# Performance work log

Hardware: AMD Instinct MI355X
Metric: run time of the kernel (lower is better)

## Reference

```python
import jax, jax.numpy as jnp
import numpy as np

G, U, I, D, L = 4, 100000, 50000, 64, 50   # graphNum, users, items, latdim, pos_length
H = 4                                       # attention heads
ATT_LAYERS = 2
SSL = 32
GNN_LAYER = 2
LEAKY = 0.5
B = 2048                                    # number of sequences
NPRED = 8192                                # scored (u,i) pairs
NS = 4096                                   # ssl samples per graph (pos half + neg half)


def leaky(x):
    return jnp.where(x >= 0, x, LEAKY * x)


def layer_norm(x, eps=1e-5):
    m = jnp.mean(x, axis=-1, keepdims=True)
    v = jnp.mean(jnp.square(x - m), axis=-1, keepdims=True)
    return (x - m) * jax.lax.rsqrt(v + eps)


def lstm(x, Wih, Whh, bih, bhh):
    # x: [N, T, D] -> [N, T, D]; torch gate order i,f,g,o
    N = x.shape[0]
    def step(carry, xt):
        h, c = carry
        g = xt @ Wih.T + h @ Whh.T + bih + bhh
        i_, f_, g_, o_ = jnp.split(g, 4, axis=-1)
        c = jax.nn.sigmoid(f_) * c + jax.nn.sigmoid(i_) * jnp.tanh(g_)
        h = jax.nn.sigmoid(o_) * jnp.tanh(c)
        return (h, c), h
    h0 = jnp.zeros((N, D), x.dtype)
    (_, _), ys = jax.lax.scan(step, (h0, h0), jnp.swapaxes(x, 0, 1))
    return jnp.swapaxes(ys, 0, 1)


def mhsa(x, Wq, Wk, Wv):
    # x: [N, T, D]; per-head scaled dot-product self-attention, heads concatenated
    N, T, Dm = x.shape
    dk = Dm // H
    q = (x @ Wq).reshape(N, T, H, dk)
    k = (x @ Wk).reshape(N, T, H, dk)
    v = (x @ Wv).reshape(N, T, H, dk)
    s = jnp.einsum('nthd,nshd->nhts', q, k) / jnp.sqrt(jnp.asarray(dk, x.dtype))
    a = jax.nn.softmax(s, axis=-1)
    return jnp.einsum('nhts,nshd->nthd', a, v).reshape(N, T, Dm)


def setup_inputs() -> dict:
    key = jax.random.key(0)
    ks = iter(jax.random.split(key, 40))
    W = 0.05  # weight init scale keeps attention logits / lstm gates in sane range
    def n(shape, scale=1.0):
        return jax.random.normal(next(ks), shape, jnp.float32) * scale
    return dict(
        uEmbed=n((G, U, D), W), iEmbed=n((G, I, D), W), posEmbed=n((L, D), W),
        Wih=n((4 * D, D), W), Whh=n((4 * D, D), W),
        bih=jnp.zeros((4 * D,), jnp.float32), bhh=jnp.zeros((4 * D,), jnp.float32),
        Wq0=n((D, D), W), Wk0=n((D, D), W), Wv0=n((D, D), W),
        Wq1=n((D, D), W), Wk1=n((D, D), W), Wv1=n((D, D), W),
        Wq_seq=n((ATT_LAYERS, D, D), W), Wk_seq=n((ATT_LAYERS, D, D), W), Wv_seq=n((ATT_LAYERS, D, D), W),
        meta2_W=n((SSL, 3 * D), W), meta2_b=jnp.zeros((SSL,), jnp.float32),
        meta3_W=n((1, SSL), W), meta3_b=jnp.zeros((1,), jnp.float32),
        mask=jax.random.uniform(next(ks), (B, L), jnp.float32),
        uids=jax.random.randint(next(ks), (NPRED,), 0, U),
        iids=jax.random.randint(next(ks), (NPRED,), 0, I),
        sequence=jax.random.randint(next(ks), (B, L), 0, I),
        uLocs_seq=jax.random.randint(next(ks), (NPRED,), 0, B),
        suids=jax.random.randint(next(ks), (G, NS), 0, U),
        siids=jax.random.randint(next(ks), (G, NS), 0, I),
    )


def reference(uEmbed, iEmbed, posEmbed, Wih, Whh, bih, bhh,
              Wq0, Wk0, Wv0, Wq1, Wk1, Wv1, Wq_seq, Wk_seq, Wv_seq,
              meta2_W, meta2_b, meta3_W, meta3_b, mask,
              uids, iids, sequence, uLocs_seq, suids, siids):
    # GNN loop: in this source messagePropagate returns leaky_relu(zeros) == 0,
    # so each layer appends embs[-1] unchanged and sum(embs) == (gnn_layer+1)*base.
    user_vector = (GNN_LAYER + 1) * uEmbed   # [G, U, D]
    item_vector = (GNN_LAYER + 1) * iEmbed   # [G, I, D]

    uvt = lstm(jnp.transpose(user_vector, (1, 0, 2)), Wih, Whh, bih, bhh)  # [U, G, D]
    ivt = lstm(jnp.transpose(item_vector, (1, 0, 2)), Wih, Whh, bih, bhh)  # [I, G, D]
    final_user = jnp.mean(mhsa(layer_norm(uvt), Wq0, Wk0, Wv0), axis=1)    # [U, D]
    final_item = jnp.mean(mhsa(layer_norm(ivt), Wq1, Wk1, Wv1), axis=1)    # [I, D]
    iEmbed_att = final_item

    seq_emb = iEmbed_att[sequence]                        # [B, L, D]
    m = mask[:, None, :]                                  # [B, 1, L]  (bmm reduces seq axis)
    sb = layer_norm(jnp.einsum('bol,bld->bod', m, seq_emb)
                    + jnp.einsum('bol,ld->bod', m, posEmbed))  # [B, 1, D]
    att = sb
    for i in range(ATT_LAYERS):
        a1 = mhsa(layer_norm(att), Wq_seq[i], Wk_seq[i], Wv_seq[i])
        att = leaky(a1) + att
    att_user = jnp.sum(att, axis=1)                       # [B, D]

    preds = jnp.sum(final_user[uids] * final_item[iids], axis=-1)
    preds = preds + jnp.sum(leaky(att_user[uLocs_seq]) * iEmbed_att[iids], axis=-1)

    # per-graph user weights (meta network), vectorized over graphNum
    fu = jnp.broadcast_to(final_user[None], user_vector.shape)            # [G, U, D]
    meta1 = jnp.concatenate([fu * user_vector, fu, user_vector], axis=-1)  # [G, U, 3D]
    meta2 = leaky(jnp.einsum('gud,od->guo', meta1, meta2_W) + meta2_b)
    user_weight = jax.nn.sigmoid(jnp.einsum('guo,ko->guk', meta2, meta3_W) + meta3_b)[..., 0]  # [G, U]

    S = NS // 2
    pu = final_user[suids]                                # [G, NS, D]
    pi = final_item[siids]
    w = jnp.take_along_axis(user_weight, suids, axis=1)   # [G, NS]
    S_final = jnp.sum(leaky(pu * pi), axis=-1)            # [G, NS]
    posF = jax.lax.stop_gradient(S_final[:, :S])
    negF = jax.lax.stop_gradient(S_final[:, S:])
    Sf = w[:, :S] * posF - w[:, S:] * negF
    puv = jnp.take_along_axis(user_vector, suids[..., None], axis=1)  # [G, NS, D]
    piv = jnp.take_along_axis(item_vector, siids[..., None], axis=1)
    p1 = jnp.sum(leaky(puv * piv), axis=-1)
    sslloss = jnp.sum(jnp.maximum(1.0 - Sf * (p1[:, :S] - p1[:, S:]), 0.0))
    return preds, sslloss
```

## Files before the change

kernel.cpp:

```cpp
#include <hip/hip_runtime.h>
#include <hip/hip_bf16.h>
#include <math.h>

#define G_CNT 4
#define U_CNT 100000
#define I_CNT 50000
#define N_ROWS (U_CNT + I_CNT)
#define D_DIM 64
#define T_STEPS 4
#define L_SEQ 50
#define B_CNT 2048
#define NPRED 8192
#define NS_CNT 4096
#define LEAKY_A 0.5f

typedef short bf16x8 __attribute__((ext_vector_type(8)));
typedef float f32x4 __attribute__((ext_vector_type(4)));

union U16B { unsigned u[4]; bf16x8 v; };

__device__ __forceinline__ unsigned bfr(float x) {
    unsigned u = __float_as_uint(x);
    return (u + 0x7fffu + ((u >> 16) & 1u)) >> 16;
}
__device__ __forceinline__ unsigned pkbf(float a, float b) {
    return bfr(a) | (bfr(b) << 16);
}
__device__ __forceinline__ float bf_lo(unsigned u) { return __uint_as_float(u << 16); }
__device__ __forceinline__ float bf_hi(unsigned u) { return __uint_as_float(u & 0xffff0000u); }

__device__ __forceinline__ float bcast(float v, int srcLane) {
    return __int_as_float(__builtin_amdgcn_readlane(__float_as_int(v), srcLane));
}

__device__ __forceinline__ float waveReduceSum(float v) {
    v += __shfl_xor(v, 1, 64);
    v += __shfl_xor(v, 2, 64);
    v += __shfl_xor(v, 4, 64);
    v += __shfl_xor(v, 8, 64);
    v += __shfl_xor(v, 16, 64);
    v += __shfl_xor(v, 32, 64);
    return v;
}

__device__ __forceinline__ float waveLayerNorm(float v) {
    float s  = waveReduceSum(v);
    float s2 = waveReduceSum(v * v);
    float mean = s * (1.0f / 64.0f);
    float var  = s2 * (1.0f / 64.0f) - mean * mean;
    return (v - mean) * rsqrtf(var + 1e-5f);
}

__device__ __forceinline__ float rcp_(float x) { return __builtin_amdgcn_rcpf(x); }

__device__ __forceinline__ float sigm(float x) { return rcp_(1.0f + __expf(-x)); }
__device__ __forceinline__ float tanh_(float x) {
    float xc = fminf(x, 15.0f);
    float t = __expf(2.0f * xc);
    return (t - 1.0f) * rcp_(t + 1.0f);
}
__device__ __forceinline__ float leakyf(float x) { return x >= 0.0f ? x : LEAKY_A * x; }

__device__ __forceinline__ int gate_perm(int m, int p) {
    int ty = m >> 2, mm = m & 3;
    return ty * 64 + 32 * (mm >> 1) + 8 * (p >> 2) + 4 * (mm & 1) + (p & 3);
}

__global__ __launch_bounds__(512)
void prep_kernel(const float* __restrict__ Wih, const float* __restrict__ Whh,
                 const float* __restrict__ bih, const float* __restrict__ bhh,
                 const float* __restrict__ Wq0, const float* __restrict__ Wk0, const float* __restrict__ Wv0,
                 const float* __restrict__ Wq1, const float* __restrict__ Wk1, const float* __restrict__ Wv1,
                 char* __restrict__ fragtab, float* __restrict__ biastab)
{
    const int tid  = threadIdx.x;
    const int lane = tid & 63;
    const int wave = tid >> 6;
    const int r    = lane & 15;
    const int g    = lane >> 4;

#pragma unroll
    for (int i = 0; i < 8; ++i) {
        int f = wave * 8 + i;
        int m = f >> 2, kc = f & 3;
        int gate = gate_perm(m, r);
        int k0 = kc * 32 + 8 * g;
        const bool isX = (k0 < 64);
        const float sc = isX ? 3.0f : 1.0f;
        const float* src = isX ? (Wih + gate * 64 + k0)
                               : (Whh + gate * 64 + (k0 - 64));
        float4 lo = *(const float4*)src;
        float4 hi = *(const float4*)(src + 4);
        U16B u;
        u.u[0] = pkbf(sc * lo.x, sc * lo.y); u.u[1] = pkbf(sc * lo.z, sc * lo.w);
        u.u[2] = pkbf(sc * hi.x, sc * hi.y); u.u[3] = pkbf(sc * hi.z, sc * hi.w);
        *(bf16x8*)(fragtab + f * 1024 + lane * 16) = u.v;
    }
#pragma unroll
    for (int i = 0; i < 6; ++i) {
        int f = 64 + i * 8 + wave;
        int m = (wave >> 1) & 3, kc = wave & 1;
        const float* WM = (i == 0) ? Wq0 : (i == 1) ? Wk0 : (i == 2) ? Wv0
                        : (i == 3) ? Wq1 : (i == 4) ? Wk1 : Wv1;
        int dp = m * 16 + r;
        int k0 = kc * 32 + 8 * g;
        float v0 = WM[(k0 + 0) * 64 + dp], v1 = WM[(k0 + 1) * 64 + dp];
        float v2 = WM[(k0 + 2) * 64 + dp], v3 = WM[(k0 + 3) * 64 + dp];
        float v4 = WM[(k0 + 4) * 64 + dp], v5 = WM[(k0 + 5) * 64 + dp];
        float v6 = WM[(k0 + 6) * 64 + dp], v7 = WM[(k0 + 7) * 64 + dp];
        U16B u;
        u.u[0] = pkbf(v0, v1); u.u[1] = pkbf(v2, v3);
        u.u[2] = pkbf(v4, v5); u.u[3] = pkbf(v6, v7);
        *(bf16x8*)(fragtab + f * 1024 + lane * 16) = u.v;
    }
    if (tid < 256) {
        int m = tid >> 4, p = tid & 15;
        int gate = gate_perm(m, p);
        biastab[tid] = bih[gate] + bhh[gate];
    }
}

__global__ __launch_bounds__(512)
void tower_kernel(const float* __restrict__ uEmbed, const float* __restrict__ iEmbed,
                  const char* __restrict__ fragtab, const float* __restrict__ biastab,
                  float* __restrict__ finalv)
{
    __shared__ char WFRAG[65536];
    __shared__ char XNF[65536];
    __shared__ float BSL[256];

    const int tid  = threadIdx.x;
    const int lane = tid & 63;
    const int wave = tid >> 6;
    const int r    = lane & 15;
    const int g    = lane >> 4;

#pragma unroll
    for (int i = 0; i < 8; ++i) {
        int off = (wave * 8 + i) * 1024 + lane * 16;
        *(bf16x8*)(WFRAG + off) = *(const bf16x8*)(fragtab + off);
    }
    if (tid < 256) BSL[tid] = biastab[tid];
    __syncthreads();

    const int rowBase0 = blockIdx.x * 128 + wave * 16;
    const bool active  = rowBase0 < N_ROWS;
    const int rowBase  = active ? rowBase0 : (N_ROWS - 16);
    const bool isUser = rowBase < U_CNT;
    const float* emb = isUser ? uEmbed : iEmbed;
    const int cnt = isUser ? U_CNT : I_CNT;
    const int rloc = (isUser ? rowBase : rowBase - U_CNT) + r;

    char* xnfw = XNF + wave * 8192;

    float cst[4][4];
#pragma unroll
    for (int mm = 0; mm < 4; ++mm)
#pragma unroll
        for (int rg = 0; rg < 4; ++rg) cst[mm][rg] = 0.0f;

    uint2 hp4[4];

#pragma unroll
    for (int t = 0; t < 4; ++t) {
        bf16x8 xft[2];
#pragma unroll
        for (int c = 0; c < 2; ++c) {
            const float* p = emb + ((size_t)t * cnt + rloc) * 64 + c * 32 + 8 * g;
            float4 lo = *(const float4*)p;
            float4 hi = *(const float4*)(p + 4);
            U16B u;
            u.u[0] = pkbf(lo.x, lo.y);
            u.u[1] = pkbf(lo.z, lo.w);
            u.u[2] = pkbf(hi.x, hi.y);
            u.u[3] = pkbf(hi.z, hi.w);
            xft[c] = u.v;
        }
        bf16x8 hfr[2];
        if (t > 0) {
#pragma unroll
            for (int c = 0; c < 2; ++c) {
                U16B u;
                u.u[0] = hp4[2 * c].x;     u.u[1] = hp4[2 * c].y;
                u.u[2] = hp4[2 * c + 1].x; u.u[3] = hp4[2 * c + 1].y;
                hfr[c] = u.v;
            }
        }
        __builtin_amdgcn_sched_barrier(0);

#pragma unroll
        for (int mm = 0; mm < 4; ++mm) {
            f32x4 acc[4];
#pragma unroll
            for (int ty = 0; ty < 4; ++ty)
                acc[ty] = *(const f32x4*)((const char*)BSL + (ty * 4 + mm) * 64 + g * 16);
#pragma unroll
            for (int kc = 0; kc < 2; ++kc)
#pragma unroll
                for (int ty = 0; ty < 4; ++ty) {
                    bf16x8 af = *(const bf16x8*)(WFRAG + ((ty * 4 + mm) * 4 + kc) * 1024 + lane * 16);
                    acc[ty] = __builtin_amdgcn_mfma_f32_16x16x32_bf16(af, xft[kc], acc[ty], 0, 0, 0);
                }
            if (t > 0) {
#pragma unroll
                for (int c = 0; c < 2; ++c)
#pragma unroll
                    for (int ty = 0; ty < 4; ++ty) {
                        bf16x8 af = *(const bf16x8*)(WFRAG + ((ty * 4 + mm) * 4 + 2 + c) * 1024 + lane * 16);
                        acc[ty] = __builtin_amdgcn_mfma_f32_16x16x32_bf16(af, hfr[c], acc[ty], 0, 0, 0);
                    }
            }
            float hv[4];
#pragma unroll
            for (int rg = 0; rg < 4; ++rg) {
                float cc = sigm(acc[1][rg]) * cst[mm][rg] + sigm(acc[0][rg]) * tanh_(acc[2][rg]);
                cst[mm][rg] = cc;
                hv[rg] = sigm(acc[3][rg]) * tanh_(cc);
            }
            hp4[mm].x = pkbf(hv[0], hv[1]);
            hp4[mm].y = pkbf(hv[2], hv[3]);
            __builtin_amdgcn_sched_barrier(0);
        }

        {
            float hv[16];
#pragma unroll
            for (int mm = 0; mm < 4; ++mm) {
                hv[mm * 4 + 0] = bf_lo(hp4[mm].x); hv[mm * 4 + 1] = bf_hi(hp4[mm].x);
                hv[mm * 4 + 2] = bf_lo(hp4[mm].y); hv[mm * 4 + 3] = bf_hi(hp4[mm].y);
            }
            float s = 0.f, s2 = 0.f;
#pragma unroll
            for (int i2 = 0; i2 < 16; ++i2) { s += hv[i2]; s2 += hv[i2] * hv[i2]; }
            s  += __shfl_xor(s, 16, 64);  s  += __shfl_xor(s, 32, 64);
            s2 += __shfl_xor(s2, 16, 64); s2 += __shfl_xor(s2, 32, 64);
            float mean = s * (1.f / 64.f);
            float var  = s2 * (1.f / 64.f) - mean * mean;
            float rs = rsqrtf(var + 1e-5f);
            uint2 xp[4];
#pragma unroll
            for (int mm = 0; mm < 4; ++mm) {
                float x0 = (hv[mm * 4 + 0] - mean) * rs, x1 = (hv[mm * 4 + 1] - mean) * rs;
                float x2 = (hv[mm * 4 + 2] - mean) * rs, x3 = (hv[mm * 4 + 3] - mean) * rs;
                xp[mm].x = pkbf(x0, x1); xp[mm].y = pkbf(x2, x3);
            }
#pragma unroll
            for (int c = 0; c < 2; ++c) {
                U16B u;
                u.u[0] = xp[2 * c].x;     u.u[1] = xp[2 * c].y;
                u.u[2] = xp[2 * c + 1].x; u.u[3] = xp[2 * c + 1].y;
                *(bf16x8*)(xnfw + t * 2048 + c * 1024 + lane * 16) = u.v;
            }
        }
        __builtin_amdgcn_sched_barrier(0);
    }

    const int base3 = isUser ? 0 : 3;
    float* dst = finalv + (size_t)(rowBase + r) * 64;

#pragma unroll
    for (int mm = 0; mm < 4; ++mm) {
        bf16x8 fq[2], fk[2], fv[2];
#pragma unroll
        for (int kc = 0; kc < 2; ++kc) {
            fq[kc] = *(const bf16x8*)(fragtab + (size_t)(64 + (0 + base3) * 8 + mm * 2 + kc) * 1024 + lane * 16);
            fk[kc] = *(const bf16x8*)(fragtab + (size_t)(64 + (1 + base3) * 8 + mm * 2 + kc) * 1024 + lane * 16);
            fv[kc] = *(const bf16x8*)(fragtab + (size_t)(64 + (2 + base3) * 8 + mm * 2 + kc) * 1024 + lane * 16);
        }
        float q[4][4], k[4][4], v[4][4];
#pragma unroll
        for (int t = 0; t < 4; ++t) {
            f32x4 aq = {0.f, 0.f, 0.f, 0.f};
            f32x4 ak = {0.f, 0.f, 0.f, 0.f};
            f32x4 av = {0.f, 0.f, 0.f, 0.f};
#pragma unroll
            for (int kc = 0; kc < 2; ++kc) {
                bf16x8 xn = *(const bf16x8*)(xnfw + t * 2048 + kc * 1024 + lane * 16);
                aq = __builtin_amdgcn_mfma_f32_16x16x32_bf16(fq[kc], xn, aq, 0, 0, 0);
                ak = __builtin_amdgcn_mfma_f32_16x16x32_bf16(fk[kc], xn, ak, 0, 0, 0);
                av = __builtin_amdgcn_mfma_f32_16x16x32_bf16(fv[kc], xn, av, 0, 0, 0);
            }
#pragma unroll
            for (int rg = 0; rg < 4; ++rg) {
                q[t][rg] = aq[rg]; k[t][rg] = ak[rg]; v[t][rg] = av[rg];
            }
            __builtin_amdgcn_sched_barrier(0);
        }
        float sc[4][4];
#pragma unroll
        for (int t = 0; t < 4; ++t)
#pragma unroll
            for (int s5 = 0; s5 < 4; ++s5) {
                float pr = q[t][0] * k[s5][0] + q[t][1] * k[s5][1]
                         + q[t][2] * k[s5][2] + q[t][3] * k[s5][3];
                pr += __shfl_xor(pr, 16, 64);
                pr += __shfl_xor(pr, 32, 64);
                sc[t][s5] = pr * 0.25f;
            }
        float o0 = 0.f, o1 = 0.f, o2 = 0.f, o3 = 0.f;
#pragma unroll
        for (int t = 0; t < 4; ++t) {
            float mx = fmaxf(fmaxf(sc[t][0], sc[t][1]), fmaxf(sc[t][2], sc[t][3]));
            float e0 = __expf(sc[t][0] - mx), e1 = __expf(sc[t][1] - mx);
            float e2 = __expf(sc[t][2] - mx), e3 = __expf(sc[t][3] - mx);
            float inv = rcp_(e0 + e1 + e2 + e3);
            float a0 = e0 * inv, a1 = e1 * inv, a2 = e2 * inv, a3 = e3 * inv;
            o0 += a0 * v[0][0] + a1 * v[1][0] + a2 * v[2][0] + a3 * v[3][0];
            o1 += a0 * v[0][1] + a1 * v[1][1] + a2 * v[2][1] + a3 * v[3][1];
            o2 += a0 * v[0][2] + a1 * v[1][2] + a2 * v[2][2] + a3 * v[3][2];
            o3 += a0 * v[0][3] + a1 * v[1][3] + a2 * v[2][3] + a3 * v[3][3];
        }
        if (active) {
            float4 o4 = { o0 * 0.25f, o1 * 0.25f, o2 * 0.25f, o3 * 0.25f };
            *(float4*)(dst + mm * 16 + 4 * g) = o4;
        }
        __builtin_amdgcn_sched_barrier(0);
    }
}

__global__ __launch_bounds__(256)
void seq_att_kernel(const float* __restrict__ finalv, const float* __restrict__ posEmbed,
                    const float* __restrict__ mask, const int* __restrict__ sequence,
                    const float* __restrict__ Wv_seq, float* __restrict__ att_user)
{
    const int lane = threadIdx.x & 63, wave = threadIdx.x >> 6;
    const int b = blockIdx.x * 4 + wave;
    if (b >= B_CNT) return;
    const float* fitem = finalv + (size_t)U_CNT * D_DIM;

    float acc = 0.0f;
    for (int l = 0; l < L_SEQ; ++l) {
        int   sid = sequence[b * L_SEQ + l];
        float m   = mask[b * L_SEQ + l];
        acc += m * (fitem[(size_t)sid * D_DIM + lane] + posEmbed[l * D_DIM + lane]);
    }
    float att = waveLayerNorm(acc);
#pragma unroll
    for (int layer = 0; layer < 2; ++layer) {
        float xnv = waveLayerNorm(att);
        float vv = 0.0f;
        const float* Wv = Wv_seq + layer * 64 * 64;
        for (int j = 0; j < 64; ++j)
            vv = fmaf(bcast(xnv, j), Wv[j * 64 + lane], vv);
        att = leakyf(vv) + att;
    }
    att_user[b * D_DIM + lane] = att;
}

__global__ __launch_bounds__(256)
void preds_kernel(const float* __restrict__ finalv, const float* __restrict__ att_user,
                  const int* __restrict__ uids, const int* __restrict__ iids,
                  const int* __restrict__ uLocs, float* __restrict__ out)
{
    const int lane = threadIdx.x & 63, wave = threadIdx.x >> 6;
    const int n = blockIdx.x * 4 + wave;
    if (n >= NPRED) return;
    const int u = uids[n], it = iids[n], loc = uLocs[n];
    float fi = finalv[(size_t)(U_CNT + it) * D_DIM + lane];
    float fu = finalv[(size_t)u * D_DIM + lane];
    float au = leakyf(att_user[loc * D_DIM + lane]);
    float p = waveReduceSum(fu * fi + au * fi);
    if (lane == 0) out[n] = p;
}

__global__ __launch_bounds__(256)
void pergs_kernel(const float* __restrict__ finalv,
                  const float* __restrict__ uEmbed, const float* __restrict__ iEmbed,
                  const int* __restrict__ suids, const int* __restrict__ siids,
                  const float* __restrict__ W2, const float* __restrict__ b2,
                  const float* __restrict__ W3, const float* __restrict__ b3,
                  float* __restrict__ uw, float* __restrict__ SfB, float* __restrict__ p1B)
{
    const int lane = threadIdx.x & 63, wave = threadIdx.x >> 6;
    const int idx = blockIdx.x * 4 + wave;
    if (idx >= G_CNT * NS_CNT) return;
    const int g  = idx >> 12;
    const int su = suids[idx], si = siids[idx];

    float fu = finalv[(size_t)su * D_DIM + lane];
    float fi = finalv[(size_t)(U_CNT + si) * D_DIM + lane];
    float uv = 3.0f * uEmbed[((size_t)g * U_CNT + su) * D_DIM + lane];
    float iv = 3.0f * iEmbed[((size_t)g * I_CNT + si) * D_DIM + lane];

    float sf = waveReduceSum(leakyf(fu * fi));
    float pp = waveReduceSum(leakyf(uv * iv));

    float m1a = fu * uv;
    float acc3 = 0.0f;
    for (int o = 0; o < 32; ++o) {
        float part = m1a * W2[o * 192 + lane]
                   + fu  * W2[o * 192 + 64 + lane]
                   + uv  * W2[o * 192 + 128 + lane];
        part = waveReduceSum(part);
        float m2 = leakyf(part + b2[o]);
        acc3 = fmaf(m2, W3[o], acc3);
    }
    float w = rcp_(1.0f + __expf(-(acc3 + b3[0])));
    if (lane == 0) { uw[idx] = w; SfB[idx] = sf; p1B[idx] = pp; }
}

__global__ __launch_bounds__(1024)
void ssl_kernel(const float* __restrict__ uw, const float* __restrict__ SfB,
                const float* __restrict__ p1B, float* __restrict__ out)
{
    const int tid = threadIdx.x;
    float local = 0.0f;
    for (int p = tid; p < G_CNT * 2048; p += 1024) {
        int g = p >> 11, s = p & 2047;
        int ip = g * NS_CNT + s, in_ = ip + 2048;
        float Sf   = uw[ip] * SfB[ip] - uw[in_] * SfB[in_];
        float diff = p1B[ip] - p1B[in_];
        local += fmaxf(1.0f - Sf * diff, 0.0f);
    }
    local = waveReduceSum(local);
    __shared__ float part[16];
    const int wave = tid >> 6, lane = tid & 63;
    if (lane == 0) part[wave] = local;
    __syncthreads();
    if (tid == 0) {
        float s = 0.0f;
        for (int i = 0; i < 16; ++i) s += part[i];
        out[NPRED] = s;
    }
}

extern "C" void kernel_launch(void* const* d_in, const int* in_sizes, int n_in,
                              void* d_out, int out_size, void* d_ws, size_t ws_size,
                              hipStream_t stream)
{
    const float* uEmbed  = (const float*)d_in[0];
    const float* iEmbed  = (const float*)d_in[1];
    const float* posEmbed= (const float*)d_in[2];
    const float* Wih     = (const float*)d_in[3];
    const float* Whh     = (const float*)d_in[4];
    const float* bih     = (const float*)d_in[5];
    const float* bhh     = (const float*)d_in[6];
    const float* Wq0     = (const float*)d_in[7];
    const float* Wk0     = (const float*)d_in[8];
    const float* Wv0     = (const float*)d_in[9];
    const float* Wq1     = (const float*)d_in[10];
    const float* Wk1     = (const float*)d_in[11];
    const float* Wv1     = (const float*)d_in[12];
    const float* Wv_seq  = (const float*)d_in[15];
    const float* meta2_W = (const float*)d_in[16];
    const float* meta2_b = (const float*)d_in[17];
    const float* meta3_W = (const float*)d_in[18];
    const float* meta3_b = (const float*)d_in[19];
    const float* mask    = (const float*)d_in[20];
    const int*   uids    = (const int*)d_in[21];
    const int*   iids    = (const int*)d_in[22];
    const int*   sequence= (const int*)d_in[23];
    const int*   uLocs   = (const int*)d_in[24];
    const int*   suids   = (const int*)d_in[25];
    const int*   siids   = (const int*)d_in[26];

    char*  wsB      = (char*)d_ws;
    char*  fragtab  = wsB;
    float* biastab  = (float*)(wsB + 116 * 1024);
    float* finalv   = (float*)(wsB + 128 * 1024);
    float* att_user = finalv + (size_t)N_ROWS * D_DIM;
    float* uwB      = att_user + (size_t)B_CNT * D_DIM;
    float* SfB      = uwB + (size_t)G_CNT * NS_CNT;
    float* p1B      = SfB + (size_t)G_CNT * NS_CNT;
    float* out      = (float*)d_out;

    prep_kernel<<<1, 512, 0, stream>>>(
        Wih, Whh, bih, bhh, Wq0, Wk0, Wv0, Wq1, Wk1, Wv1, fragtab, biastab);

    tower_kernel<<<(N_ROWS + 127) / 128, 512, 0, stream>>>(
        uEmbed, iEmbed, fragtab, biastab, finalv);

    seq_att_kernel<<<(B_CNT + 3) / 4, 256, 0, stream>>>(
        finalv, posEmbed, mask, sequence, Wv_seq, att_user);

    pergs_kernel<<<(G_CNT * NS_CNT) / 4, 256, 0, stream>>>(
        finalv, uEmbed, iEmbed, suids, siids, meta2_W, meta2_b, meta3_W, meta3_b,
        uwB, SfB, p1B);

    preds_kernel<<<NPRED / 4, 256, 0, stream>>>(finalv, att_user, uids, iids, uLocs, out);

    ssl_kernel<<<1, 1024, 0, stream>>>(uwB, SfB, p1B, out);
}
```

Baseline: 198.3 us.

## Split tower kernel per side, prefetch next-step embeddings, stage QKV fragments in LDS

The tower kernel becomes a template with separate user and item launches, so the side, row count and weight offset are compile-time constants. Each timestep's embedding row is now loaded one step ahead into registers, so global load latency overlaps with the LSTM MFMA work. The attention Q/K/V weight fragments are staged once per block into a new 24 KB shared buffer instead of being read from global memory per wave. In exchange, LDS use rises to about 153 KB per block, register pressure goes up, and there is an extra kernel launch with its own tail block.

New measurement: 250.6 us. +26.4%, slower.

```diff
diff --git a/kernel.cpp b/kernel.cpp
--- a/kernel.cpp
+++ b/kernel.cpp
@@ -120,12 +120,14 @@
     }
 }
 
+template <bool IS_USER>
 __global__ __launch_bounds__(512)
-void tower_kernel(const float* __restrict__ uEmbed, const float* __restrict__ iEmbed,
+void tower_kernel(const float* __restrict__ embAll,
                   const char* __restrict__ fragtab, const float* __restrict__ biastab,
                   float* __restrict__ finalv)
 {
     __shared__ char WFRAG[65536];
+    __shared__ char QFRAG[24576];
     __shared__ char XNF[65536];
     __shared__ float BSL[256];
 
@@ -135,21 +137,27 @@
     const int r    = lane & 15;
     const int g    = lane >> 4;
 
+    constexpr int SIDE_ROWS = IS_USER ? U_CNT : I_CNT;
+    constexpr int BASE3     = IS_USER ? 0 : 3;
+
 #pragma unroll
     for (int i = 0; i < 8; ++i) {
         int off = (wave * 8 + i) * 1024 + lane * 16;
         *(bf16x8*)(WFRAG + off) = *(const bf16x8*)(fragtab + off);
     }
+#pragma unroll
+    for (int i = 0; i < 3; ++i) {
+        int off = (wave * 3 + i) * 1024 + lane * 16;
+        *(bf16x8*)(QFRAG + off) =
+            *(const bf16x8*)(fragtab + (size_t)(64 + BASE3 * 8) * 1024 + off);
+    }
     if (tid < 256) BSL[tid] = biastab[tid];
     __syncthreads();
 
     const int rowBase0 = blockIdx.x * 128 + wave * 16;
-    const bool active  = rowBase0 < N_ROWS;
-    const int rowBase  = active ? rowBase0 : (N_ROWS - 16);
-    const bool isUser = rowBase < U_CNT;
-    const float* emb = isUser ? uEmbed : iEmbed;
-    const int cnt = isUser ? U_CNT : I_CNT;
-    const int rloc = (isUser ? rowBase : rowBase - U_CNT) + r;
+    const bool active  = rowBase0 < SIDE_ROWS;
+    const int rowBase  = active ? rowBase0 : (SIDE_ROWS - 16);
+    const int rloc     = rowBase + r;
 
     char* xnfw = XNF + wave * 8192;
 
@@ -160,21 +168,34 @@
         for (int rg = 0; rg < 4; ++rg) cst[mm][rg] = 0.0f;
 
     uint2 hp4[4];
+
+    float4 rlo[2], rhi[2];
+#pragma unroll
+    for (int c = 0; c < 2; ++c) {
+        const float* p = embAll + (size_t)rloc * 64 + c * 32 + 8 * g;
+        rlo[c] = *(const float4*)p;
+        rhi[c] = *(const float4*)(p + 4);
+    }
 
 #pragma unroll
     for (int t = 0; t < 4; ++t) {
         bf16x8 xft[2];
 #pragma unroll
         for (int c = 0; c < 2; ++c) {
-            const float* p = emb + ((size_t)t * cnt + rloc) * 64 + c * 32 + 8 * g;
-            float4 lo = *(const float4*)p;
-            float4 hi = *(const float4*)(p + 4);
             U16B u;
-            u.u[0] = pkbf(lo.x, lo.y);
-            u.u[1] = pkbf(lo.z, lo.w);
-            u.u[2] = pkbf(hi.x, hi.y);
-            u.u[3] = pkbf(hi.z, hi.w);
+            u.u[0] = pkbf(rlo[c].x, rlo[c].y);
+            u.u[1] = pkbf(rlo[c].z, rlo[c].w);
+            u.u[2] = pkbf(rhi[c].x, rhi[c].y);
+            u.u[3] = pkbf(rhi[c].z, rhi[c].w);
             xft[c] = u.v;
+        }
+        if (t < 3) {
+#pragma unroll
+            for (int c = 0; c < 2; ++c) {
+                const float* p = embAll + ((size_t)(t + 1) * SIDE_ROWS + rloc) * 64 + c * 32 + 8 * g;
+                rlo[c] = *(const float4*)p;
+                rhi[c] = *(const float4*)(p + 4);
+            }
         }
         bf16x8 hfr[2];
         if (t > 0) {
@@ -255,17 +276,16 @@
         __builtin_amdgcn_sched_barrier(0);
     }
 
-    const int base3 = isUser ? 0 : 3;
-    float* dst = finalv + (size_t)(rowBase + r) * 64;
+    float* dst = finalv + (size_t)((IS_USER ? 0 : U_CNT) + rowBase + r) * 64;
 
 #pragma unroll
     for (int mm = 0; mm < 4; ++mm) {
         bf16x8 fq[2], fk[2], fv[2];
 #pragma unroll
         for (int kc = 0; kc < 2; ++kc) {
-            fq[kc] = *(const bf16x8*)(fragtab + (size_t)(64 + (0 + base3) * 8 + mm * 2 + kc) * 1024 + lane * 16);
-            fk[kc] = *(const bf16x8*)(fragtab + (size_t)(64 + (1 + base3) * 8 + mm * 2 + kc) * 1024 + lane * 16);
-            fv[kc] = *(const bf16x8*)(fragtab + (size_t)(64 + (2 + base3) * 8 + mm * 2 + kc) * 1024 + lane * 16);
+            fq[kc] = *(const bf16x8*)(QFRAG + (0 * 8 + mm * 2 + kc) * 1024 + lane * 16);
+            fk[kc] = *(const bf16x8*)(QFRAG + (1 * 8 + mm * 2 + kc) * 1024 + lane * 16);
+            fv[kc] = *(const bf16x8*)(QFRAG + (2 * 8 + mm * 2 + kc) * 1024 + lane * 16);
         }
         float q[4][4], k[4][4], v[4][4];
 #pragma unroll
@@ -467,8 +487,10 @@
     prep_kernel<<<1, 512, 0, stream>>>(
         Wih, Whh, bih, bhh, Wq0, Wk0, Wv0, Wq1, Wk1, Wv1, fragtab, biastab);
 
-    tower_kernel<<<(N_ROWS + 127) / 128, 512, 0, stream>>>(
-        uEmbed, iEmbed, fragtab, biastab, finalv);
+    tower_kernel<true><<<(U_CNT + 127) / 128, 512, 0, stream>>>(
+        uEmbed, fragtab, biastab, finalv);
+    tower_kernel<false><<<(I_CNT + 127) / 128, 512, 0, stream>>>(
+        iEmbed, fragtab, biastab, finalv);
 
     seq_att_kernel<<<(B_CNT + 3) / 4, 256, 0, stream>>>(
         finalv, posEmbed, mask, sequence, Wv_seq, att_user);
```
